# Kernel tuning notes

Measured on AMD Instinct MI355X. Metric: run time of the kernel, lower is better.

## Reference

```python
import jax, jax.numpy as jnp
import numpy as np
import math

B, Q, K, C, H, D = 2, 2048, 2048, 512, 8, 64  # hidden_dim*num_heads == C


def setup_inputs() -> dict:
    key = jax.random.key(0)
    ks = jax.random.split(key, 9)
    s = 0.02
    return {
        "query_data": jax.random.normal(ks[0], (B, Q, C), jnp.float32),
        "key_data": jax.random.normal(ks[1], (B, K, C), jnp.float32),
        "bias1": jax.random.normal(ks[2], (B, 1, Q, K), jnp.float32),
        "bias2": jax.random.normal(ks[3], (1, H, Q, K), jnp.float32),
        "wq": jax.random.normal(ks[4], (C, H * D), jnp.float32) * s,
        "wk": jax.random.normal(ks[5], (C, H * D), jnp.float32) * s,
        "wv": jax.random.normal(ks[6], (C, H * D), jnp.float32) * s,
        "wo": jax.random.normal(ks[7], (H * D, C), jnp.float32) * s,
        "bo": jnp.zeros((C,), jnp.float32),
        "wg": jax.random.normal(ks[8], (C, H * D), jnp.float32) * s,
        "bg": jnp.zeros((H * D,), jnp.float32),
    }


def reference(query_data, key_data, bias1, bias2, wq, wk, wv, wo, bo, wg, bg):
    # prep_qkv: project, split heads, scale q by 1/sqrt(hidden_dim)
    q = (query_data @ wq).reshape(B, Q, H, D) / math.sqrt(D)
    k = (key_data @ wk).reshape(B, K, H, D)
    v = (key_data @ wv).reshape(B, K, H, D)
    # attention: scores [B,H,Q,K] with additive biases, softmax over K
    scores = jnp.einsum("bqhd,bkhd->bhqk", q, k) + bias1 + bias2
    attn = jax.nn.softmax(scores, axis=-1)
    out = jnp.einsum("bhqk,bkhd->bqhd", attn, v)  # [B,Q,H,D]
    # wrap_up: sigmoid gate from query data, flatten heads, output proj
    g = jax.nn.sigmoid(query_data @ wg + bg).reshape(B, Q, H, D)
    out = (out * g).reshape(B, Q, H * D)
    return out @ wo + bo
```

## Files before the change

### kernel.cpp

```cpp
#include <hip/hip_runtime.h>

typedef __bf16 bf16;
typedef __bf16 bf16x8 __attribute__((ext_vector_type(8)));
typedef __bf16 bf16x4 __attribute__((ext_vector_type(4)));
typedef float f32x4 __attribute__((ext_vector_type(4)));

#define NB 2
#define NQ 2048
#define NKK 2048
#define NC 512
#define NH 8
#define ND 64
#define NM (NB*NQ)
#define SPLITS 4
#define KSPL (NKK/SPLITS)
#define NTILES (KSPL/32)
#define PLS 36

__global__ __launch_bounds__(256) void cvt_bf16_kernel(const float* __restrict__ in,
                                                       bf16* __restrict__ out, int n4) {
  int i = blockIdx.x * 256 + threadIdx.x;
  if (i < n4) {
    float4 v = ((const float4*)in)[i];
    bf16x4 o;
    o[0] = (bf16)v.x; o[1] = (bf16)v.y; o[2] = (bf16)v.z; o[3] = (bf16)v.w;
    ((bf16x4*)out)[i] = o;
  }
}

__global__ __launch_bounds__(256) void transpose_w_kernel(const float* __restrict__ W,
                                                          bf16* __restrict__ WT) {
  __shared__ float t[32][33];
  int n0 = blockIdx.x * 32, k0 = blockIdx.y * 32;
  int c = threadIdx.x & 31, r0 = threadIdx.x >> 5;
  for (int r = r0; r < 32; r += 8) t[r][c] = W[(size_t)(k0 + r) * NC + n0 + c];
  __syncthreads();
  for (int r = r0; r < 32; r += 8) WT[(size_t)(n0 + r) * NC + k0 + c] = (bf16)t[c][r];
}

__global__ __launch_bounds__(256) void gemm_kernel(const bf16* __restrict__ X,
                                                   const bf16* __restrict__ WT,
                                                   const float* __restrict__ bias,
                                                   void* __restrict__ out, int epi) {
  __shared__ bf16 Xs[64][72];
  __shared__ bf16 Ws[64][72];
  int m0 = blockIdx.y * 64, n0 = blockIdx.x * 64;
  int tid = threadIdx.x, lane = tid & 63, wave = tid >> 6;
  int wm = wave >> 1, wn = wave & 1;
  int lr = lane & 15, lg = lane >> 4;
  f32x4 acc[2][2] = {};
  for (int k0 = 0; k0 < 512; k0 += 64) {
#pragma unroll
    for (int j = 0; j < 2; j++) {
      int cc = tid + 256 * j;
      int r = cc >> 3, c8 = (cc & 7) * 8;
      *(uint4*)&Xs[r][c8] = *(const uint4*)&X[(size_t)(m0 + r) * 512 + k0 + c8];
      *(uint4*)&Ws[r][c8] = *(const uint4*)&WT[(size_t)(n0 + r) * 512 + k0 + c8];
    }
    __syncthreads();
#pragma unroll
    for (int kk = 0; kk < 64; kk += 32) {
      bf16x8 a[2], b[2];
      a[0] = *(const bf16x8*)&Xs[wm * 32 + lr][kk + lg * 8];
      a[1] = *(const bf16x8*)&Xs[wm * 32 + 16 + lr][kk + lg * 8];
      b[0] = *(const bf16x8*)&Ws[wn * 32 + lr][kk + lg * 8];
      b[1] = *(const bf16x8*)&Ws[wn * 32 + 16 + lr][kk + lg * 8];
#pragma unroll
      for (int mi = 0; mi < 2; mi++)
#pragma unroll
        for (int ni = 0; ni < 2; ni++)
          acc[mi][ni] = __builtin_amdgcn_mfma_f32_16x16x32_bf16(a[mi], b[ni], acc[mi][ni], 0, 0, 0);
    }
    __syncthreads();
  }
#pragma unroll
  for (int mi = 0; mi < 2; mi++) {
#pragma unroll
    for (int ni = 0; ni < 2; ni++) {
#pragma unroll
      for (int i = 0; i < 4; i++) {
        int grow = m0 + wm * 32 + mi * 16 + lg * 4 + i;
        int gcol = n0 + wn * 32 + ni * 16 + lr;
        float v = acc[mi][ni][i];
        if (epi == 0) {
          int b = grow >> 11, q = grow & 2047, h = gcol >> 6, d = gcol & 63;
          ((bf16*)out)[((size_t)(b * NH + h) * NQ + q) * ND + d] = (bf16)(v * 0.125f);
        } else if (epi == 1 || epi == 2) {
          int b = grow >> 11, kq = grow & 2047, h = gcol >> 6, d = gcol & 63;
          ((bf16*)out)[((size_t)(b * NH + h) * NKK + kq) * ND + d] = (bf16)v;
        } else if (epi == 3) {
          v += bias[gcol];
          v = 1.0f / (1.0f + __expf(-v));
          ((float*)out)[(size_t)grow * 512 + gcol] = v;
        } else {
          ((float*)out)[(size_t)grow * 512 + gcol] = v + bias[gcol];
        }
      }
    }
  }
}

__global__ __launch_bounds__(256) void transpose_v_kernel(const bf16* __restrict__ vh,
                                                          bf16* __restrict__ vT) {
  __shared__ bf16 t[64][72];
  int bh = blockIdx.y;
  int kk0 = blockIdx.x * 64;
  const bf16* src = vh + (size_t)bh * NKK * ND;
  bf16* dst = vT + (size_t)bh * ND * NKK;
#pragma unroll
  for (int j = 0; j < 2; j++) {
    int c = threadIdx.x + 256 * j;
    int r = c >> 3, cc = (c & 7) * 8;
    *(uint4*)&t[r][cc] = *(const uint4*)&src[(size_t)(kk0 + r) * ND + cc];
  }
  __syncthreads();
#pragma unroll
  for (int j = 0; j < 2; j++) {
    int c = threadIdx.x + 256 * j;
    int d = c >> 3, ck = (c & 7) * 8;
    bf16 tmp[8];
#pragma unroll
    for (int x = 0; x < 8; x++) tmp[x] = t[ck + x][d];
    *(uint4*)&dst[(size_t)d * NKK + kk0 + ck] = *(const uint4*)tmp;
  }
}

struct Tile {
  float b1v[2][4];
  float b2v[2][4];
  bf16x8 kf[2][2];
};

__device__ __forceinline__ void load_tile(int k0, const float* __restrict__ b1,
                                          const float* __restrict__ b2,
                                          const bf16* __restrict__ Kp,
                                          int lr, int lg, Tile& T) {
#pragma unroll
  for (int f = 0; f < 2; f++) {
#pragma unroll
    for (int i = 0; i < 4; i++) {
      int row = lg * 4 + i;
      int col = k0 + f * 16 + lr;
      T.b1v[f][i] = b1[row * NKK + col];
      T.b2v[f][i] = b2[row * NKK + col];
    }
  }
#pragma unroll
  for (int f = 0; f < 2; f++) {
#pragma unroll
    for (int kc = 0; kc < 2; kc++)
      T.kf[f][kc] = *(const bf16x8*)&Kp[(size_t)(k0 + f * 16 + lr) * ND + kc * 32 + lg * 8];
  }
}

__device__ __forceinline__ void compute_tile(const Tile& T, int k0,
                                             const bf16* __restrict__ Vt,
                                             bf16x8 qf0, bf16x8 qf1,
                                             f32x4 (&o)[4], float (&lrow)[4],
                                             bf16 (*pl)[PLS], int lr, int lg) {
  bf16x8 vf0 = *(const bf16x8*)&Vt[(size_t)(0 * 16 + lr) * NKK + k0 + lg * 8];
  bf16x8 vf1 = *(const bf16x8*)&Vt[(size_t)(1 * 16 + lr) * NKK + k0 + lg * 8];
  bf16x8 vf2 = *(const bf16x8*)&Vt[(size_t)(2 * 16 + lr) * NKK + k0 + lg * 8];
  bf16x8 vf3 = *(const bf16x8*)&Vt[(size_t)(3 * 16 + lr) * NKK + k0 + lg * 8];
  f32x4 s[2];
#pragma unroll
  for (int f = 0; f < 2; f++) {
    f32x4 c;
#pragma unroll
    for (int i = 0; i < 4; i++) c[i] = T.b1v[f][i] + T.b2v[f][i];
    c = __builtin_amdgcn_mfma_f32_16x16x32_bf16(qf0, T.kf[f][0], c, 0, 0, 0);
    c = __builtin_amdgcn_mfma_f32_16x16x32_bf16(qf1, T.kf[f][1], c, 0, 0, 0);
    s[f] = c;
  }
#pragma unroll
  for (int i = 0; i < 4; i++) {
    float p0 = __expf(s[0][i]);
    float p1 = __expf(s[1][i]);
    lrow[i] += p0 + p1;
    pl[lg * 4 + i][lr] = (bf16)p0;
    pl[lg * 4 + i][16 + lr] = (bf16)p1;
  }
  bf16x8 pa = *(const bf16x8*)&pl[lr][lg * 8];
  o[0] = __builtin_amdgcn_mfma_f32_16x16x32_bf16(pa, vf0, o[0], 0, 0, 0);
  o[1] = __builtin_amdgcn_mfma_f32_16x16x32_bf16(pa, vf1, o[1], 0, 0, 0);
  o[2] = __builtin_amdgcn_mfma_f32_16x16x32_bf16(pa, vf2, o[2], 0, 0, 0);
  o[3] = __builtin_amdgcn_mfma_f32_16x16x32_bf16(pa, vf3, o[3], 0, 0, 0);
}

__global__ __launch_bounds__(512, 4) void attn_kernel(
    const bf16* __restrict__ qh, const bf16* __restrict__ kh, const bf16* __restrict__ vT,
    const float* __restrict__ bias1, const float* __restrict__ bias2,
    float* __restrict__ o_part, float* __restrict__ l_part) {
  __shared__ bf16 plds[8][16][PLS];
  int b = blockIdx.y, q0 = blockIdx.x * 16, split = blockIdx.z;
  int h = threadIdx.x >> 6, lane = threadIdx.x & 63;
  int lr = lane & 15, lg = lane >> 4;
  int kbase = split * KSPL;
  const bf16* Qp = qh + ((size_t)(b * NH + h) * NQ + q0) * ND;
  const bf16* Kp = kh + (size_t)(b * NH + h) * NKK * ND;
  const bf16* Vt = vT + (size_t)(b * NH + h) * ND * NKK;
  const float* b1 = bias1 + ((size_t)b * NQ + q0) * NKK;
  const float* b2 = bias2 + ((size_t)h * NQ + q0) * NKK;

  bf16x8 qf0 = *(const bf16x8*)&Qp[lr * 64 + lg * 8];
  bf16x8 qf1 = *(const bf16x8*)&Qp[lr * 64 + 32 + lg * 8];

  f32x4 o[4] = {};
  float lrow[4] = {0.f, 0.f, 0.f, 0.f};
  bf16(*pl)[PLS] = plds[h];

  Tile TA, TB;
  load_tile(kbase, b1, b2, Kp, lr, lg, TA);
  for (int t = 0; t < NTILES; t += 2) {
    load_tile(kbase + (t + 1) * 32, b1, b2, Kp, lr, lg, TB);
    compute_tile(TA, kbase + t * 32, Vt, qf0, qf1, o, lrow, pl, lr, lg);
    if (t + 2 < NTILES) load_tile(kbase + (t + 2) * 32, b1, b2, Kp, lr, lg, TA);
    compute_tile(TB, kbase + (t + 1) * 32, Vt, qf0, qf1, o, lrow, pl, lr, lg);
  }

  float lred[4];
#pragma unroll
  for (int i = 0; i < 4; i++) {
    float L = lrow[i];
    L += __shfl_xor(L, 1);
    L += __shfl_xor(L, 2);
    L += __shfl_xor(L, 4);
    L += __shfl_xor(L, 8);
    lred[i] = L;
  }

  float* op = o_part + (((size_t)(split * NB + b) * NH + h) * NQ + q0) * ND;
#pragma unroll
  for (int ni = 0; ni < 4; ni++)
#pragma unroll
    for (int i = 0; i < 4; i++)
      op[(lg * 4 + i) * ND + ni * 16 + lr] = o[ni][i];
  if (lr == 0) {
    float* lp = l_part + ((size_t)(split * NB + b) * NH + h) * NQ + q0;
#pragma unroll
    for (int i = 0; i < 4; i++) lp[lg * 4 + i] = lred[i];
  }
}

__global__ __launch_bounds__(256) void combine_kernel(const float* __restrict__ o_part,
                                                      const float* __restrict__ l_part,
                                                      const float* __restrict__ gate,
                                                      bf16* __restrict__ ao) {
  size_t t = (size_t)blockIdx.x * 256 + threadIdx.x;
  int d0 = (int)(t & 15) * 4;
  int h = (int)((t >> 4) & 7);
  int q = (int)((t >> 7) & 2047);
  int b = (int)(t >> 18);
  f32x4 acc = {};
  float L = 0.f;
#pragma unroll
  for (int s = 0; s < SPLITS; s++) {
    size_t base = (((size_t)(s * NB + b) * NH + h) * NQ + q);
    acc += *(const f32x4*)&o_part[base * ND + d0];
    L += l_part[base];
  }
  float inv = 1.0f / L;
  size_t gi = ((size_t)b * NQ + q) * 512 + h * 64 + d0;
  f32x4 g = *(const f32x4*)&gate[gi];
  bf16x4 r;
#pragma unroll
  for (int j = 0; j < 4; j++) r[j] = (bf16)(acc[j] * inv * g[j]);
  *(bf16x4*)&ao[gi] = r;
}

extern "C" void kernel_launch(void* const* d_in, const int* in_sizes, int n_in,
                              void* d_out, int out_size, void* d_ws, size_t ws_size,
                              hipStream_t stream) {
  const float* query = (const float*)d_in[0];
  const float* keyd  = (const float*)d_in[1];
  const float* bias1 = (const float*)d_in[2];
  const float* bias2 = (const float*)d_in[3];
  const float* wq = (const float*)d_in[4];
  const float* wk = (const float*)d_in[5];
  const float* wv = (const float*)d_in[6];
  const float* wo = (const float*)d_in[7];
  const float* bo = (const float*)d_in[8];
  const float* wg = (const float*)d_in[9];
  const float* bg = (const float*)d_in[10];

  char* ws = (char*)d_ws;
  size_t off = 0;
  auto alloc = [&](size_t bytes) {
    void* p = ws + off;
    off += (bytes + 255) & ~(size_t)255;
    return p;
  };
  bf16* qd_bf = (bf16*)alloc((size_t)NM * 512 * 2);
  bf16* kd_bf = (bf16*)alloc((size_t)NM * 512 * 2);
  bf16* wqT = (bf16*)alloc((size_t)512 * 512 * 2);
  bf16* wkT = (bf16*)alloc((size_t)512 * 512 * 2);
  bf16* wvT = (bf16*)alloc((size_t)512 * 512 * 2);
  bf16* wgT = (bf16*)alloc((size_t)512 * 512 * 2);
  bf16* woT = (bf16*)alloc((size_t)512 * 512 * 2);
  bf16* qh  = (bf16*)alloc((size_t)NB * NH * NQ * ND * 2);
  bf16* kh  = (bf16*)alloc((size_t)NB * NH * NKK * ND * 2);
  bf16* vh  = (bf16*)alloc((size_t)NB * NH * NKK * ND * 2);
  bf16* vTt = (bf16*)alloc((size_t)NB * NH * ND * NKK * 2);
  float* gbuf = (float*)alloc((size_t)NM * 512 * 4);
  bf16* aob = (bf16*)alloc((size_t)NM * 512 * 2);
  float* o_part = (float*)alloc((size_t)SPLITS * NB * NH * NQ * ND * 4);
  float* l_part = (float*)alloc((size_t)SPLITS * NB * NH * NQ * 4);

  int n4 = NM * 512 / 4;
  cvt_bf16_kernel<<<dim3(n4 / 256), 256, 0, stream>>>(query, qd_bf, n4);
  cvt_bf16_kernel<<<dim3(n4 / 256), 256, 0, stream>>>(keyd, kd_bf, n4);

  transpose_w_kernel<<<dim3(16, 16), 256, 0, stream>>>(wq, wqT);
  transpose_w_kernel<<<dim3(16, 16), 256, 0, stream>>>(wk, wkT);
  transpose_w_kernel<<<dim3(16, 16), 256, 0, stream>>>(wv, wvT);
  transpose_w_kernel<<<dim3(16, 16), 256, 0, stream>>>(wg, wgT);
  transpose_w_kernel<<<dim3(16, 16), 256, 0, stream>>>(wo, woT);

  gemm_kernel<<<dim3(8, 64), 256, 0, stream>>>(qd_bf, wqT, nullptr, qh, 0);
  gemm_kernel<<<dim3(8, 64), 256, 0, stream>>>(kd_bf, wkT, nullptr, kh, 1);
  gemm_kernel<<<dim3(8, 64), 256, 0, stream>>>(kd_bf, wvT, nullptr, vh, 2);
  gemm_kernel<<<dim3(8, 64), 256, 0, stream>>>(qd_bf, wgT, bg, gbuf, 3);

  transpose_v_kernel<<<dim3(32, 16), 256, 0, stream>>>(vh, vTt);

  attn_kernel<<<dim3(128, 2, 4), 512, 0, stream>>>(qh, kh, vTt, bias1, bias2, o_part, l_part);

  combine_kernel<<<dim3((NB * NQ * NH * 16) / 256), 256, 0, stream>>>(o_part, l_part, gbuf, aob);

  gemm_kernel<<<dim3(8, 64), 256, 0, stream>>>(aob, woT, bo, d_out, 4);
}
```

Measured before the change: 262.2 us.

## Stage attention biases through LDS with async global-to-LDS loads and remap blocks

Bias1 and bias2 tiles are now fetched cooperatively with global_load_lds directly into a double-buffered shared-memory stage, replacing per-lane scattered register loads of the biases. A __syncthreads per tile separates the stages. The grid is flattened and block indices are permuted so that consecutive blocks are spread across batch/split, likely to improve L2/XCD locality of K/V and bias reads. This adds barrier overhead and LDS pressure, and it relies on the async-copy instruction's ordering with respect to the barrier without an explicit vmcnt wait.

After: 253.0 us. 3.5% less time.

```diff
diff --git a/kernel.cpp b/kernel.cpp
--- a/kernel.cpp
+++ b/kernel.cpp
@@ -125,82 +125,34 @@
   }
 }
 
-struct Tile {
-  float b1v[2][4];
-  float b2v[2][4];
-  bf16x8 kf[2][2];
-};
-
-__device__ __forceinline__ void load_tile(int k0, const float* __restrict__ b1,
-                                          const float* __restrict__ b2,
-                                          const bf16* __restrict__ Kp,
-                                          int lr, int lg, Tile& T) {
-#pragma unroll
-  for (int f = 0; f < 2; f++) {
-#pragma unroll
-    for (int i = 0; i < 4; i++) {
-      int row = lg * 4 + i;
-      int col = k0 + f * 16 + lr;
-      T.b1v[f][i] = b1[row * NKK + col];
-      T.b2v[f][i] = b2[row * NKK + col];
-    }
-  }
-#pragma unroll
-  for (int f = 0; f < 2; f++) {
-#pragma unroll
-    for (int kc = 0; kc < 2; kc++)
-      T.kf[f][kc] = *(const bf16x8*)&Kp[(size_t)(k0 + f * 16 + lr) * ND + kc * 32 + lg * 8];
-  }
-}
-
-__device__ __forceinline__ void compute_tile(const Tile& T, int k0,
-                                             const bf16* __restrict__ Vt,
-                                             bf16x8 qf0, bf16x8 qf1,
-                                             f32x4 (&o)[4], float (&lrow)[4],
-                                             bf16 (*pl)[PLS], int lr, int lg) {
-  bf16x8 vf0 = *(const bf16x8*)&Vt[(size_t)(0 * 16 + lr) * NKK + k0 + lg * 8];
-  bf16x8 vf1 = *(const bf16x8*)&Vt[(size_t)(1 * 16 + lr) * NKK + k0 + lg * 8];
-  bf16x8 vf2 = *(const bf16x8*)&Vt[(size_t)(2 * 16 + lr) * NKK + k0 + lg * 8];
-  bf16x8 vf3 = *(const bf16x8*)&Vt[(size_t)(3 * 16 + lr) * NKK + k0 + lg * 8];
-  f32x4 s[2];
-#pragma unroll
-  for (int f = 0; f < 2; f++) {
-    f32x4 c;
-#pragma unroll
-    for (int i = 0; i < 4; i++) c[i] = T.b1v[f][i] + T.b2v[f][i];
-    c = __builtin_amdgcn_mfma_f32_16x16x32_bf16(qf0, T.kf[f][0], c, 0, 0, 0);
-    c = __builtin_amdgcn_mfma_f32_16x16x32_bf16(qf1, T.kf[f][1], c, 0, 0, 0);
-    s[f] = c;
-  }
-#pragma unroll
-  for (int i = 0; i < 4; i++) {
-    float p0 = __expf(s[0][i]);
-    float p1 = __expf(s[1][i]);
-    lrow[i] += p0 + p1;
-    pl[lg * 4 + i][lr] = (bf16)p0;
-    pl[lg * 4 + i][16 + lr] = (bf16)p1;
-  }
-  bf16x8 pa = *(const bf16x8*)&pl[lr][lg * 8];
-  o[0] = __builtin_amdgcn_mfma_f32_16x16x32_bf16(pa, vf0, o[0], 0, 0, 0);
-  o[1] = __builtin_amdgcn_mfma_f32_16x16x32_bf16(pa, vf1, o[1], 0, 0, 0);
-  o[2] = __builtin_amdgcn_mfma_f32_16x16x32_bf16(pa, vf2, o[2], 0, 0, 0);
-  o[3] = __builtin_amdgcn_mfma_f32_16x16x32_bf16(pa, vf3, o[3], 0, 0, 0);
+__device__ __forceinline__ void gload16(const float* g, float* l) {
+  __builtin_amdgcn_global_load_lds((const __attribute__((address_space(1))) void*)g,
+                                   (__attribute__((address_space(3))) void*)l, 16, 0, 0);
+}
+__device__ __forceinline__ void gload4(const float* g, float* l) {
+  __builtin_amdgcn_global_load_lds((const __attribute__((address_space(1))) void*)g,
+                                   (__attribute__((address_space(3))) void*)l, 4, 0, 0);
 }
 
 __global__ __launch_bounds__(512, 4) void attn_kernel(
     const bf16* __restrict__ qh, const bf16* __restrict__ kh, const bf16* __restrict__ vT,
     const float* __restrict__ bias1, const float* __restrict__ bias2,
     float* __restrict__ o_part, float* __restrict__ l_part) {
+  __shared__ float b1s[2][16 * 32];
+  __shared__ float b2s[2][8 * 16 * 32];
   __shared__ bf16 plds[8][16][PLS];
-  int b = blockIdx.y, q0 = blockIdx.x * 16, split = blockIdx.z;
-  int h = threadIdx.x >> 6, lane = threadIdx.x & 63;
+  int l = blockIdx.x;
+  int idx = (l & 7) * 128 + (l >> 3);
+  int q0 = (idx & 127) * 16;
+  int r = idx >> 7;
+  int b = r & 1, split = r >> 1;
+  int tid = threadIdx.x;
+  int h = tid >> 6, lane = tid & 63;
   int lr = lane & 15, lg = lane >> 4;
   int kbase = split * KSPL;
   const bf16* Qp = qh + ((size_t)(b * NH + h) * NQ + q0) * ND;
   const bf16* Kp = kh + (size_t)(b * NH + h) * NKK * ND;
   const bf16* Vt = vT + (size_t)(b * NH + h) * ND * NKK;
-  const float* b1 = bias1 + ((size_t)b * NQ + q0) * NKK;
-  const float* b2 = bias2 + ((size_t)h * NQ + q0) * NKK;
 
   bf16x8 qf0 = *(const bf16x8*)&Qp[lr * 64 + lg * 8];
   bf16x8 qf1 = *(const bf16x8*)&Qp[lr * 64 + 32 + lg * 8];
@@ -209,14 +161,64 @@
   float lrow[4] = {0.f, 0.f, 0.f, 0.f};
   bf16(*pl)[PLS] = plds[h];
 
-  Tile TA, TB;
-  load_tile(kbase, b1, b2, Kp, lr, lg, TA);
-  for (int t = 0; t < NTILES; t += 2) {
-    load_tile(kbase + (t + 1) * 32, b1, b2, Kp, lr, lg, TB);
-    compute_tile(TA, kbase + t * 32, Vt, qf0, qf1, o, lrow, pl, lr, lg);
-    if (t + 2 < NTILES) load_tile(kbase + (t + 2) * 32, b1, b2, Kp, lr, lg, TA);
-    compute_tile(TB, kbase + (t + 1) * 32, Vt, qf0, qf1, o, lrow, pl, lr, lg);
-  }
+#define STAGE(c, s)                                                              \
+  do {                                                                           \
+    int kcol = kbase + (c) * 32;                                                 \
+    _Pragma("unroll")                                                            \
+    for (int j = 0; j < 2; j++) {                                                \
+      int uu = tid + j * 512;                                                    \
+      int h_ = uu >> 7, row_ = (uu >> 3) & 15, c4 = (uu & 7) * 4;                \
+      gload16(bias2 + ((size_t)h_ * NQ + q0 + row_) * NKK + kcol + c4,           \
+              &b2s[s][uu * 4]);                                                  \
+    }                                                                            \
+    int row1 = tid >> 5, col1 = tid & 31;                                        \
+    gload4(bias1 + ((size_t)b * NQ + q0 + row1) * NKK + kcol + col1,             \
+           &b1s[s][tid]);                                                        \
+  } while (0)
+
+  STAGE(0, 0);
+  __syncthreads();
+
+  for (int t = 0; t < NTILES; t++) {
+    int s = t & 1;
+    if (t + 1 < NTILES) STAGE(t + 1, s ^ 1);
+    int k0 = kbase + t * 32;
+    bf16x8 vf0 = *(const bf16x8*)&Vt[(size_t)(0 * 16 + lr) * NKK + k0 + lg * 8];
+    bf16x8 vf1 = *(const bf16x8*)&Vt[(size_t)(1 * 16 + lr) * NKK + k0 + lg * 8];
+    bf16x8 vf2 = *(const bf16x8*)&Vt[(size_t)(2 * 16 + lr) * NKK + k0 + lg * 8];
+    bf16x8 vf3 = *(const bf16x8*)&Vt[(size_t)(3 * 16 + lr) * NKK + k0 + lg * 8];
+    f32x4 sv[2];
+#pragma unroll
+    for (int f = 0; f < 2; f++) {
+      const bf16* kp = Kp + (size_t)(k0 + f * 16 + lr) * ND + lg * 8;
+      bf16x8 kfa = *(const bf16x8*)kp;
+      bf16x8 kfb = *(const bf16x8*)(kp + 32);
+      f32x4 c;
+#pragma unroll
+      for (int i = 0; i < 4; i++) {
+        int off = (lg * 4 + i) * 32 + f * 16 + lr;
+        c[i] = b1s[s][off] + b2s[s][h * 512 + off];
+      }
+      c = __builtin_amdgcn_mfma_f32_16x16x32_bf16(qf0, kfa, c, 0, 0, 0);
+      c = __builtin_amdgcn_mfma_f32_16x16x32_bf16(qf1, kfb, c, 0, 0, 0);
+      sv[f] = c;
+    }
+#pragma unroll
+    for (int i = 0; i < 4; i++) {
+      float p0 = __expf(sv[0][i]);
+      float p1 = __expf(sv[1][i]);
+      lrow[i] += p0 + p1;
+      pl[lg * 4 + i][lr] = (bf16)p0;
+      pl[lg * 4 + i][16 + lr] = (bf16)p1;
+    }
+    bf16x8 pa = *(const bf16x8*)&pl[lr][lg * 8];
+    o[0] = __builtin_amdgcn_mfma_f32_16x16x32_bf16(pa, vf0, o[0], 0, 0, 0);
+    o[1] = __builtin_amdgcn_mfma_f32_16x16x32_bf16(pa, vf1, o[1], 0, 0, 0);
+    o[2] = __builtin_amdgcn_mfma_f32_16x16x32_bf16(pa, vf2, o[2], 0, 0, 0);
+    o[3] = __builtin_amdgcn_mfma_f32_16x16x32_bf16(pa, vf3, o[3], 0, 0, 0);
+    __syncthreads();
+  }
+#undef STAGE
 
   float lred[4];
 #pragma unroll
@@ -323,7 +325,7 @@
 
   transpose_v_kernel<<<dim3(32, 16), 256, 0, stream>>>(vh, vTt);
 
-  attn_kernel<<<dim3(128, 2, 4), 512, 0, stream>>>(qh, kh, vTt, bias1, bias2, o_part, l_part);
+  attn_kernel<<<dim3(1024), 512, 0, stream>>>(qh, kh, vTt, bias1, bias2, o_part, l_part);
 
   combine_kernel<<<dim3((NB * NQ * NH * 16) / 256), 256, 0, stream>>>(o_part, l_part, gbuf, aob);
 
```
